# Kernel optimization log

Hardware: AMD Instinct MI355X
Metric: run time of the kernel (lower is better)

The kernel has to match this reference:

```python
import jax, jax.numpy as jnp
import numpy as np

B, D, C_IN, C_OUT = 256, 8, 2, 4


def setup_inputs() -> dict:
    key = jax.random.key(0)
    k1, k2, k3, k4 = jax.random.split(key, 4)
    rho = jax.random.normal(k1, (B, C_IN * D * D, C_IN * D * D), dtype=jnp.float32)
    ux = jax.random.normal(k2, (D, D), dtype=jnp.float32)
    uy = jax.random.normal(k3, (D, D), dtype=jnp.float32)
    uc = jax.random.normal(k4, (C_OUT, C_OUT), dtype=jnp.float32)
    return {"rho": rho, "ux": ux, "uy": uy, "uc": uc}


def _insert_channels(rho, d, c_in, c_out):
    # Faithful port of _InsertChannels: move each (channel f, pixel i,j) row/col
    # index to channel f + (c_out - c_in) in the enlarged register.
    b = rho.shape[0]
    x = jnp.arange(c_in * d * d)
    f = x // (d * d)                       # channel index
    i = (x % (d * d)) // d                 # row pixel
    j = x % d                              # col pixel
    new_idx = i * d + j + (f + (c_out - c_in)) * d * d  # [c_in*d^2]
    big = jnp.zeros((b, c_out * d * d, c_out * d * d), dtype=rho.dtype)
    # Indices are a bijection onto a sub-block, so add == set (matches
    # index_put_(..., accumulate=True) in torch).
    return big.at[:, new_idx[:, None], new_idx[None, :]].add(rho)


def reference(rho, ux, uy, uc):
    d = ux.shape[0]
    c_out = uc.shape[0]
    c_in = rho.shape[1] // (d * d)
    # channel insertion (c_in < c_out path)
    rho_big = _insert_channels(rho, d, c_in, c_out)        # [b, C, C], C = c_out*d^2
    # u = kron(uc, kron(ux, uy))
    u = jnp.kron(uc, jnp.kron(ux, uy))                     # [C, C]
    # new_rho = u @ rho @ u^H (real float32 -> conj is identity, transpose only)
    u_rho = jnp.einsum('pq,bqr->bpr', u, rho_big)
    new_rho = jnp.einsum('bpr,sr->bps', u_rho, u)
    return new_rho
```

## Files before the change

### kernel.cpp

```cpp
#include <hip/hip_runtime.h>


#define TPB 512

__global__ __launch_bounds__(TPB, 2) void qconv_fused(
    const float* __restrict__ rho,
    const float* __restrict__ ux,
    const float* __restrict__ uy,
    const float* __restrict__ uc,
    float* __restrict__ out)
{
    __shared__ alignas(16) float L[4][64][68];

    const int tid  = threadIdx.x;
    const int b    = blockIdx.x;
    const int w    = tid >> 6;
    const int lane = tid & 63;
    const int pyp  = lane >> 3, qyp = lane & 7;

    const int qg  = tid & 15;
    const int csh = (tid >> 4) & 1;
    const int spl = tid >> 5;

    float e0[4], e1[4];
#pragma unroll
    for (int c = 0; c < 4; ++c) { e0[c] = uc[c*4+2]; e1[c] = uc[c*4+3]; }
    float* ob = out + (size_t)b * 65536;

    float Y[64];

    if (w < 4) {
        const int c1 = w >> 1, c2 = w & 1;
        const int px = lane >> 3, qx = lane & 7;
        const float* rb = rho + (size_t)b * 16384
                        + (size_t)((c1 << 6) + (px << 3)) * 128 + (c2 << 6) + (qx << 3);

        float X[64];
#pragma unroll
        for (int py = 0; py < 8; ++py) {
            float4 lo = *(const float4*)(rb + py * 128);
            float4 hi = *(const float4*)(rb + py * 128 + 4);
            X[py*8+0]=lo.x; X[py*8+1]=lo.y; X[py*8+2]=lo.z; X[py*8+3]=lo.w;
            X[py*8+4]=hi.x; X[py*8+5]=hi.y; X[py*8+6]=hi.z; X[py*8+7]=hi.w;
        }
#pragma unroll
        for (int py = 0; py < 8; ++py)
#pragma unroll
            for (int j = 0; j < 8; ++j) {
                float acc = 0.f;
#pragma unroll
                for (int k = 0; k < 8; ++k) acc += uy[j*8+k] * X[py*8+k];
                Y[py*8+j] = acc;
            }
#pragma unroll
        for (int i = 0; i < 8; ++i)
#pragma unroll
            for (int j = 0; j < 8; ++j) {
                float acc = 0.f;
#pragma unroll
                for (int k = 0; k < 8; ++k) acc += uy[i*8+k] * Y[k*8+j];
                X[i*8+j] = acc;
            }
#pragma unroll
        for (int e = 0; e < 64; ++e) L[w][e][lane] = X[e];
        __asm__ volatile("s_waitcnt lgkmcnt(0)" ::: "memory");
#pragma unroll
        for (int f4 = 0; f4 < 16; ++f4) {
            float4 v = *(const float4*)&L[w][lane][f4 * 4];
            X[f4*4+0]=v.x; X[f4*4+1]=v.y; X[f4*4+2]=v.z; X[f4*4+3]=v.w;
        }
#pragma unroll
        for (int p = 0; p < 8; ++p)
#pragma unroll
            for (int j = 0; j < 8; ++j) {
                float acc = 0.f;
#pragma unroll
                for (int k = 0; k < 8; ++k) acc += ux[j*8+k] * X[p*8+k];
                Y[p*8+j] = acc;
            }
    }

#pragma unroll
    for (int s = 0; s < 4; ++s) {
        if (w < 4) {
#pragma unroll
            for (int i2 = 0; i2 < 2; ++i2) {
                const int i = 2*s + i2;
#pragma unroll
                for (int j = 0; j < 8; ++j) {
                    float acc = 0.f;
#pragma unroll
                    for (int k = 0; k < 8; ++k) acc += ux[i*8+k] * Y[k*8+j];
                    L[w][i*8+pyp][j*8+qyp] = acc;
                }
            }
        }
        __syncthreads();

        const int sp = 16*s + spl;
        float4 wv[4];
#pragma unroll
        for (int ww = 0; ww < 4; ++ww) wv[ww] = *(const float4*)&L[ww][sp][qg * 4];
#pragma unroll
        for (int c = 0; c < 4; ++c) {
#pragma unroll
            for (int cs2 = 0; cs2 < 2; ++cs2) {
                const int cs = 2*csh + cs2;
                const float k00 = e0[c]*e0[cs], k01 = e0[c]*e1[cs];
                const float k10 = e1[c]*e0[cs], k11 = e1[c]*e1[cs];
                float4 v;
                v.x = k00*wv[0].x + k01*wv[1].x + k10*wv[2].x + k11*wv[3].x;
                v.y = k00*wv[0].y + k01*wv[1].y + k10*wv[2].y + k11*wv[3].y;
                v.z = k00*wv[0].z + k01*wv[1].z + k10*wv[2].z + k11*wv[3].z;
                v.w = k00*wv[0].w + k01*wv[1].w + k10*wv[2].w + k11*wv[3].w;
                *(float4*)&ob[(size_t)((c*64 + sp) * 256 + cs*64 + qg*4)] = v;
            }
        }
    }
}

extern "C" void kernel_launch(void* const* d_in, const int* in_sizes, int n_in,
                              void* d_out, int out_size, void* d_ws, size_t ws_size,
                              hipStream_t stream) {
    const float* rho = (const float*)d_in[0];
    const float* ux  = (const float*)d_in[1];
    const float* uy  = (const float*)d_in[2];
    const float* uc  = (const float*)d_in[3];
    float* out = (float*)d_out;
    qconv_fused<<<dim3(256), dim3(TPB), 0, stream>>>(rho, ux, uy, uc, out);
}
```

Baseline: 88.86 us.

## Cut register use with in-place transforms, swizzle LDS transpose, nontemporal stores

Removes the second 64-float register array by doing each 8x8 transform in place through small temporaries, which lowers VGPR pressure. Adds an XOR swizzle to the LDS transpose to cut bank conflicts. Replaces __syncthreads with an explicit lgkmcnt wait plus s_barrier. Writes output with nontemporal stores to avoid polluting cache. These are several independent tweaks; the swizzle must stay consistent between writer and reader, and the weaker barrier relies on no global-memory ordering being needed across it.

```diff
diff --git a/kernel.cpp b/kernel.cpp
--- a/kernel.cpp
+++ b/kernel.cpp
@@ -2,6 +2,8 @@
 
 
 #define TPB 512
+
+typedef float nfloat4 __attribute__((ext_vector_type(4)));
 
 __global__ __launch_bounds__(TPB, 2) void qconv_fused(
     const float* __restrict__ rho,
@@ -27,7 +29,7 @@
     for (int c = 0; c < 4; ++c) { e0[c] = uc[c*4+2]; e1[c] = uc[c*4+3]; }
     float* ob = out + (size_t)b * 65536;
 
-    float Y[64];
+    float X[64];
 
     if (w < 4) {
         const int c1 = w >> 1, c2 = w & 1;
@@ -35,7 +37,6 @@
         const float* rb = rho + (size_t)b * 16384
                         + (size_t)((c1 << 6) + (px << 3)) * 128 + (c2 << 6) + (qx << 3);
 
-        float X[64];
 #pragma unroll
         for (int py = 0; py < 8; ++py) {
             float4 lo = *(const float4*)(rb + py * 128);
@@ -43,41 +44,61 @@
             X[py*8+0]=lo.x; X[py*8+1]=lo.y; X[py*8+2]=lo.z; X[py*8+3]=lo.w;
             X[py*8+4]=hi.x; X[py*8+5]=hi.y; X[py*8+6]=hi.z; X[py*8+7]=hi.w;
         }
+
 #pragma unroll
-        for (int py = 0; py < 8; ++py)
+        for (int r = 0; r < 8; ++r) {
+            float t[8];
 #pragma unroll
             for (int j = 0; j < 8; ++j) {
-                float acc = 0.f;
+                float a = 0.f;
 #pragma unroll
-                for (int k = 0; k < 8; ++k) acc += uy[j*8+k] * X[py*8+k];
-                Y[py*8+j] = acc;
+                for (int k = 0; k < 8; ++k) a += uy[j*8+k] * X[r*8+k];
+                t[j] = a;
             }
 #pragma unroll
-        for (int i = 0; i < 8; ++i)
+            for (int j = 0; j < 8; ++j) X[r*8+j] = t[j];
+        }
+
+#pragma unroll
+        for (int cc = 0; cc < 8; ++cc) {
+            float t[8];
+#pragma unroll
+            for (int i = 0; i < 8; ++i) {
+                float a = 0.f;
+#pragma unroll
+                for (int k = 0; k < 8; ++k) a += uy[i*8+k] * X[k*8+cc];
+                t[i] = a;
+            }
+#pragma unroll
+            for (int i = 0; i < 8; ++i) X[i*8+cc] = t[i];
+        }
+
+#pragma unroll
+        for (int e = 0; e < 64; ++e)
+            L[w][e][lane ^ (((e >> 3) & 7) << 2)] = X[e];
+        __asm__ volatile("s_waitcnt lgkmcnt(0)" ::: "memory");
+        {
+            const int sw = ((lane >> 3) & 7) << 2;
+#pragma unroll
+            for (int f4 = 0; f4 < 16; ++f4) {
+                float4 v = *(const float4*)&L[w][lane][(f4 * 4) ^ sw];
+                X[f4*4+0]=v.x; X[f4*4+1]=v.y; X[f4*4+2]=v.z; X[f4*4+3]=v.w;
+            }
+        }
+
+#pragma unroll
+        for (int p = 0; p < 8; ++p) {
+            float t[8];
 #pragma unroll
             for (int j = 0; j < 8; ++j) {
-                float acc = 0.f;
+                float a = 0.f;
 #pragma unroll
-                for (int k = 0; k < 8; ++k) acc += uy[i*8+k] * Y[k*8+j];
-                X[i*8+j] = acc;
+                for (int k = 0; k < 8; ++k) a += ux[j*8+k] * X[p*8+k];
+                t[j] = a;
             }
 #pragma unroll
-        for (int e = 0; e < 64; ++e) L[w][e][lane] = X[e];
-        __asm__ volatile("s_waitcnt lgkmcnt(0)" ::: "memory");
-#pragma unroll
-        for (int f4 = 0; f4 < 16; ++f4) {
-            float4 v = *(const float4*)&L[w][lane][f4 * 4];
-            X[f4*4+0]=v.x; X[f4*4+1]=v.y; X[f4*4+2]=v.z; X[f4*4+3]=v.w;
+            for (int j = 0; j < 8; ++j) X[p*8+j] = t[j];
         }
-#pragma unroll
-        for (int p = 0; p < 8; ++p)
-#pragma unroll
-            for (int j = 0; j < 8; ++j) {
-                float acc = 0.f;
-#pragma unroll
-                for (int k = 0; k < 8; ++k) acc += ux[j*8+k] * X[p*8+k];
-                Y[p*8+j] = acc;
-            }
     }
 
 #pragma unroll
@@ -90,12 +111,14 @@
                 for (int j = 0; j < 8; ++j) {
                     float acc = 0.f;
 #pragma unroll
-                    for (int k = 0; k < 8; ++k) acc += ux[i*8+k] * Y[k*8+j];
+                    for (int k = 0; k < 8; ++k) acc += ux[i*8+k] * X[k*8+j];
                     L[w][i*8+pyp][j*8+qyp] = acc;
                 }
             }
         }
-        __syncthreads();
+        __asm__ volatile("s_waitcnt lgkmcnt(0)" ::: "memory");
+        __builtin_amdgcn_s_barrier();
+        __asm__ volatile("" ::: "memory");
 
         const int sp = 16*s + spl;
         float4 wv[4];
@@ -108,12 +131,13 @@
                 const int cs = 2*csh + cs2;
                 const float k00 = e0[c]*e0[cs], k01 = e0[c]*e1[cs];
                 const float k10 = e1[c]*e0[cs], k11 = e1[c]*e1[cs];
-                float4 v;
+                nfloat4 v;
                 v.x = k00*wv[0].x + k01*wv[1].x + k10*wv[2].x + k11*wv[3].x;
                 v.y = k00*wv[0].y + k01*wv[1].y + k10*wv[2].y + k11*wv[3].y;
                 v.z = k00*wv[0].z + k01*wv[1].z + k10*wv[2].z + k11*wv[3].z;
                 v.w = k00*wv[0].w + k01*wv[1].w + k10*wv[2].w + k11*wv[3].w;
-                *(float4*)&ob[(size_t)((c*64 + sp) * 256 + cs*64 + qg*4)] = v;
+                __builtin_nontemporal_store(v,
+                    (nfloat4*)&ob[(size_t)((c*64 + sp) * 256 + cs*64 + qg*4)]);
             }
         }
     }
```

Measured after the change: 89.97 us. No clear change (+1.2%).
